# Performance work log

Hardware: AMD Instinct MI355X
Metric: run time of the kernel (lower is better)

Reference implementation:

```python
import jax, jax.numpy as jnp
import numpy as np

AGENT_SIZE = 64
NEIGH_SIZE = 64
NUM_HEAD = 4
MID_SIZE = 32
N_AGENT = 200000
HM = NUM_HEAD * MID_SIZE  # 128
OUT = HM // 2             # 64


def _xavier(key, shape):
    fan_in, fan_out = shape[0], shape[1]
    std = (2.0 / (fan_in + fan_out)) ** 0.5
    return jax.random.normal(key, shape, dtype=jnp.float32) * std


def setup_inputs() -> dict:
    key = jax.random.key(0)
    ks = jax.random.split(key, 12)
    agent = jax.random.normal(ks[0], (N_AGENT, AGENT_SIZE), dtype=jnp.float32)
    neighbor = jax.random.normal(ks[1], (N_AGENT, 4, NEIGH_SIZE), dtype=jnp.float32)
    neighbor_mask = jax.random.randint(ks[2], (N_AGENT, 4), 0, 2, dtype=jnp.int32)
    return {
        "agent": agent,
        "neighbor": neighbor,
        "neighbor_mask": neighbor_mask,
        "W_agent": _xavier(ks[3], (AGENT_SIZE, HM)),
        "b_agent": jnp.zeros((HM,), jnp.float32),
        "W_neigh": _xavier(ks[4], (NEIGH_SIZE, HM)),
        "b_neigh": jnp.zeros((HM,), jnp.float32),
        "W_hid": _xavier(ks[5], (NEIGH_SIZE, HM)),
        "b_hid": jnp.zeros((HM,), jnp.float32),
        "W_out": _xavier(ks[6], (HM, OUT)),
        "b_out": jnp.zeros((OUT,), jnp.float32),
    }


def reference(agent, neighbor, neighbor_mask,
              W_agent, b_agent, W_neigh, b_neigh,
              W_hid, b_hid, W_out, b_out):
    n = agent.shape[0]
    mask = neighbor_mask.astype(jnp.float32)  # [n, 4], 1 = masked
    # linear + relu projections
    a = jax.nn.relu(agent @ W_agent + b_agent).reshape(n, NUM_HEAD, MID_SIZE)          # [n,h,m]
    nr = jax.nn.relu(neighbor @ W_neigh + b_neigh).reshape(n, 4, NUM_HEAD, MID_SIZE)   # [n,4,h,m]
    nh = jax.nn.relu(neighbor @ W_hid + b_hid).reshape(n, 4, NUM_HEAD, MID_SIZE)       # [n,4,h,m]
    # attention logits: agent . neighbor per head -> [n, h, 4]
    att = jnp.einsum('nhm,nkhm->nhk', a, nr)
    att_score = jax.nn.softmax(mask[:, None, :] * -1e8 + att, axis=-1)                 # [n,h,4]
    att_score = (1.0 - mask[:, None, :]) * att_score
    # weighted MEAN over the 4 neighbors (faithful to .mean(2))
    out = jnp.einsum('nhk,nkhm->nhm', att_score, nh) / 4.0                              # [n,h,m]
    out = out.reshape(n, HM)
    return jax.nn.relu(out @ W_out + b_out)
```

## Files before the change

### kernel.cpp

```cpp
#include <hip/hip_runtime.h>
#include <cstdint>


typedef _Float16 f16;
typedef f16 f16x8 __attribute__((ext_vector_type(8)));
typedef float f32x4 __attribute__((ext_vector_type(4)));

#define MFMA(a, b, c) __builtin_amdgcn_mfma_f32_16x16x32_f16(a, b, c, 0, 0, 0)

__device__ __forceinline__ f16x8 ld_cvt8(const float* __restrict__ p) {
    float4 a = *(const float4*)p;
    float4 b = *(const float4*)(p + 4);
    f16x8 r;
    r[0] = (f16)a.x; r[1] = (f16)a.y; r[2] = (f16)a.z; r[3] = (f16)a.w;
    r[4] = (f16)b.x; r[5] = (f16)b.y; r[6] = (f16)b.z; r[7] = (f16)b.w;
    return r;
}

__device__ __forceinline__ float rowsum16(float x) {
    x += __int_as_float(__builtin_amdgcn_update_dpp(0, __float_as_int(x), 0x128, 0xf, 0xf, true));
    x += __int_as_float(__builtin_amdgcn_update_dpp(0, __float_as_int(x), 0x124, 0xf, 0xf, true));
    x += __int_as_float(__builtin_amdgcn_update_dpp(0, __float_as_int(x), 0x122, 0xf, 0xf, true));
    x += __int_as_float(__builtin_amdgcn_update_dpp(0, __float_as_int(x), 0x121, 0xf, 0xf, true));
    return x;
}

__global__ void prep_w(const float* __restrict__ Wa, const float* __restrict__ Wn,
                       const float* __restrict__ Wh, const float* __restrict__ Wo,
                       f16* __restrict__ ws) {
    int i = blockIdx.x * 256 + threadIdx.x;
    int m = i >> 13;
    int j = i & 8191;
    if (m < 3) {
        const float* W = (m == 0) ? Wa : ((m == 1) ? Wn : Wh);
        int n = j >> 6, k = j & 63;
        ws[m * 8192 + j] = (f16)W[k * 128 + n];
    } else {
        int n = j >> 7, k = j & 127;
        ws[24576 + j] = (f16)Wo[k * 64 + n];
    }
}

__global__ __launch_bounds__(256, 4)
void gat_mfma(const float* __restrict__ agent,
              const float* __restrict__ neighbor,
              const int*   __restrict__ nmask,
              const f16*   __restrict__ ws,
              const float* __restrict__ ba, const float* __restrict__ bn,
              const float* __restrict__ bh, const float* __restrict__ bo,
              float* __restrict__ out)
{
    __shared__ float mneg[256];
    __shared__ f16   ot[64 * 136];

    const int tid  = threadIdx.x;
    const int lane = tid & 63;
    const int h    = __builtin_amdgcn_readfirstlane(tid >> 6);
    const int l15  = lane & 15;
    const int q    = lane >> 4;
    const long base = (long)blockIdx.x * 64;

    mneg[tid] = -1e8f * (float)nmask[base * 4 + tid];

    const float bav[2] = { ba[h * 32 + l15], ba[h * 32 + 16 + l15] };
    const float bnv[2] = { bn[h * 32 + l15], bn[h * 32 + 16 + l15] };
    const float bhv[2] = { bh[h * 32 + l15], bh[h * 32 + 16 + l15] };
    const float bov    = bo[h * 16 + l15];

    const f16* wsn = ws + 8192;
    const f16* wsh = ws + 16384;
    const f16* wso = ws + 24576;

    f16x8 wn[2][2], wh[2][2];
    #pragma unroll
    for (int ct = 0; ct < 2; ++ct)
        #pragma unroll
        for (int ks = 0; ks < 2; ++ks) {
            int n = h * 32 + ct * 16 + l15;
            wn[ct][ks] = *(const f16x8*)(wsn + n * 64 + ks * 32 + q * 8);
            wh[ct][ks] = *(const f16x8*)(wsh + n * 64 + ks * 32 + q * 8);
        }

    __syncthreads();

    #pragma unroll 1
    for (int rt = 0; rt < 4; ++rt) {
        f32x4 p0 = {0.f, 0.f, 0.f, 0.f}, p1 = {0.f, 0.f, 0.f, 0.f};
        {
            const float* ap = agent + (base + rt * 16 + l15) * 64 + q * 8;
            f16x8 a0 = ld_cvt8(ap);
            f16x8 a1 = ld_cvt8(ap + 32);
            #pragma unroll
            for (int ct = 0; ct < 2; ++ct) {
                f16x8 w0 = *(const f16x8*)(ws + (h * 32 + ct * 16 + l15) * 64 + q * 8);
                f16x8 w1 = *(const f16x8*)(ws + (h * 32 + ct * 16 + l15) * 64 + 32 + q * 8);
                f32x4 c = {0.f, 0.f, 0.f, 0.f};
                c = MFMA(a0, w0, c);
                c = MFMA(a1, w1, c);
                if (ct == 0) p0 = c; else p1 = c;
            }
            #pragma unroll
            for (int r = 0; r < 4; ++r) {
                p0[r] = fmaxf(p0[r] + bav[0], 0.f);
                p1[r] = fmaxf(p1[r] + bav[1], 0.f);
            }
        }

        f32x4 o0 = {0.f, 0.f, 0.f, 0.f}, o1 = {0.f, 0.f, 0.f, 0.f};
        f32x4 ls = {0.f, 0.f, 0.f, 0.f};
        #pragma unroll
        for (int k = 0; k < 4; ++k) {
            const float* nb = neighbor + ((base + rt * 16 + l15) * 4 + k) * 64 + q * 8;
            f16x8 a0 = ld_cvt8(nb);
            f16x8 a1 = ld_cvt8(nb + 32);
            f32x4 n0 = {0.f,0.f,0.f,0.f}, n1 = {0.f,0.f,0.f,0.f};
            f32x4 h0 = {0.f,0.f,0.f,0.f}, h1 = {0.f,0.f,0.f,0.f};
            n0 = MFMA(a0, wn[0][0], n0); n0 = MFMA(a1, wn[0][1], n0);
            n1 = MFMA(a0, wn[1][0], n1); n1 = MFMA(a1, wn[1][1], n1);
            h0 = MFMA(a0, wh[0][0], h0); h0 = MFMA(a1, wh[0][1], h0);
            h1 = MFMA(a0, wh[1][0], h1); h1 = MFMA(a1, wh[1][1], h1);
            #pragma unroll
            for (int r = 0; r < 4; ++r) {
                n0[r] = fmaxf(n0[r] + bnv[0], 0.f);
                n1[r] = fmaxf(n1[r] + bnv[1], 0.f);
                h0[r] = fmaxf(h0[r] + bhv[0], 0.f);
                h1[r] = fmaxf(h1[r] + bhv[1], 0.f);
            }
            #pragma unroll
            for (int r = 0; r < 4; ++r) {
                float tp = p0[r] * n0[r] + p1[r] * n1[r];
                float logit = rowsum16(tp);
                float s = logit + mneg[(rt * 16 + q * 4 + r) * 4 + k];
                float e = __expf(s);
                ls[r] += e;
                float ep = (s > -1e7f) ? e : 0.f;
                o0[r] += ep * h0[r];
                o1[r] += ep * h1[r];
            }
        }

        #pragma unroll
        for (int r = 0; r < 4; ++r) {
            float inv = 0.25f / (ls[r] + 1e-30f);
            int row = rt * 16 + q * 4 + r;
            ot[row * 136 + h * 32 + l15]      = (f16)(o0[r] * inv);
            ot[row * 136 + h * 32 + 16 + l15] = (f16)(o1[r] * inv);
        }
    }
    __syncthreads();

    f16x8 wof[4];
    #pragma unroll
    for (int ks = 0; ks < 4; ++ks)
        wof[ks] = *(const f16x8*)(wso + (h * 16 + l15) * 128 + ks * 32 + q * 8);
    #pragma unroll
    for (int rt = 0; rt < 4; ++rt) {
        f32x4 y = {0.f, 0.f, 0.f, 0.f};
        #pragma unroll
        for (int ks = 0; ks < 4; ++ks) {
            f16x8 of = *(const f16x8*)(ot + (rt * 16 + l15) * 136 + ks * 32 + q * 8);
            y = MFMA(of, wof[ks], y);
        }
        #pragma unroll
        for (int r = 0; r < 4; ++r)
            out[(base + rt * 16 + q * 4 + r) * 64 + h * 16 + l15] = fmaxf(y[r] + bov, 0.f);
    }
}

extern "C" void kernel_launch(void* const* d_in, const int* in_sizes, int n_in,
                              void* d_out, int out_size, void* d_ws, size_t ws_size,
                              hipStream_t stream) {
    const float* agent    = (const float*)d_in[0];
    const float* neighbor = (const float*)d_in[1];
    const int*   nmask    = (const int*)d_in[2];
    const float* Wa = (const float*)d_in[3];
    const float* ba = (const float*)d_in[4];
    const float* Wn = (const float*)d_in[5];
    const float* bn = (const float*)d_in[6];
    const float* Wh = (const float*)d_in[7];
    const float* bh = (const float*)d_in[8];
    const float* Wo = (const float*)d_in[9];
    const float* bo = (const float*)d_in[10];
    float* out = (float*)d_out;
    f16* ws = (f16*)d_ws;

    prep_w<<<128, 256, 0, stream>>>(Wa, Wn, Wh, Wo, ws);

    const int n = in_sizes[0] / 64;
    const int blocks = n / 64;
    gat_mfma<<<blocks, 256, 0, stream>>>(agent, neighbor, nmask, ws,
                                         ba, bn, bh, bo, out);
}
```

Before: 421.5 us.

## Stage agent and neighbor tiles cooperatively through swizzled LDS with register prefetch

After: 472.3 us. 12.0% more time.

```diff
diff --git a/kernel.cpp b/kernel.cpp
--- a/kernel.cpp
+++ b/kernel.cpp
@@ -4,18 +4,10 @@
 
 typedef _Float16 f16;
 typedef f16 f16x8 __attribute__((ext_vector_type(8)));
+typedef f16 f16x4 __attribute__((ext_vector_type(4)));
 typedef float f32x4 __attribute__((ext_vector_type(4)));
 
 #define MFMA(a, b, c) __builtin_amdgcn_mfma_f32_16x16x32_f16(a, b, c, 0, 0, 0)
-
-__device__ __forceinline__ f16x8 ld_cvt8(const float* __restrict__ p) {
-    float4 a = *(const float4*)p;
-    float4 b = *(const float4*)(p + 4);
-    f16x8 r;
-    r[0] = (f16)a.x; r[1] = (f16)a.y; r[2] = (f16)a.z; r[3] = (f16)a.w;
-    r[4] = (f16)b.x; r[5] = (f16)b.y; r[6] = (f16)b.z; r[7] = (f16)b.w;
-    return r;
-}
 
 __device__ __forceinline__ float rowsum16(float x) {
     x += __int_as_float(__builtin_amdgcn_update_dpp(0, __float_as_int(x), 0x128, 0xf, 0xf, true));
@@ -41,6 +33,10 @@
     }
 }
 
+__device__ __forceinline__ int swz(int row, int col) {
+    return row * 64 + (col ^ ((row & 7) << 3));
+}
+
 __global__ __launch_bounds__(256, 4)
 void gat_mfma(const float* __restrict__ agent,
               const float* __restrict__ neighbor,
@@ -51,6 +47,8 @@
               float* __restrict__ out)
 {
     __shared__ float mneg[256];
+    __shared__ f16   sa[16 * 64];
+    __shared__ f16   sn[64 * 64];
     __shared__ f16   ot[64 * 136];
 
     const int tid  = threadIdx.x;
@@ -81,28 +79,61 @@
             wh[ct][ks] = *(const f16x8*)(wsh + n * 64 + ks * 32 + q * 8);
         }
 
-    __syncthreads();
+    const int sr  = tid >> 4;
+    const int sc4 = (tid & 15) * 4;
+    const float* agp = agent    + base * 64;
+    const float* nbp = neighbor + base * 4 * 64;
+
+    float4 ra = *(const float4*)(agp + tid * 4);
+    float4 rn4[4];
+    #pragma unroll
+    for (int i = 0; i < 4; ++i)
+        rn4[i] = *(const float4*)(nbp + i * 1024 + tid * 4);
 
     #pragma unroll 1
     for (int rt = 0; rt < 4; ++rt) {
-        f32x4 p0 = {0.f, 0.f, 0.f, 0.f}, p1 = {0.f, 0.f, 0.f, 0.f};
+        __syncthreads();
+
+        f16x8 wa[2][2];
+        #pragma unroll
+        for (int ct = 0; ct < 2; ++ct)
+            #pragma unroll
+            for (int ks = 0; ks < 2; ++ks)
+                wa[ct][ks] = *(const f16x8*)(ws + (h * 32 + ct * 16 + l15) * 64 + ks * 32 + q * 8);
+
         {
-            const float* ap = agent + (base + rt * 16 + l15) * 64 + q * 8;
-            f16x8 a0 = ld_cvt8(ap);
-            f16x8 a1 = ld_cvt8(ap + 32);
-            #pragma unroll
-            for (int ct = 0; ct < 2; ++ct) {
-                f16x8 w0 = *(const f16x8*)(ws + (h * 32 + ct * 16 + l15) * 64 + q * 8);
-                f16x8 w1 = *(const f16x8*)(ws + (h * 32 + ct * 16 + l15) * 64 + 32 + q * 8);
-                f32x4 c = {0.f, 0.f, 0.f, 0.f};
-                c = MFMA(a0, w0, c);
-                c = MFMA(a1, w1, c);
-                if (ct == 0) p0 = c; else p1 = c;
-            }
+            f16x4 va = { (f16)ra.x, (f16)ra.y, (f16)ra.z, (f16)ra.w };
+            *(f16x4*)&sa[swz(sr, sc4)] = va;
+            #pragma unroll
+            for (int i = 0; i < 4; ++i) {
+                int rg = i * 16 + sr;
+                int lr = (rg & 3) * 16 + (rg >> 2);
+                f16x4 v = { (f16)rn4[i].x, (f16)rn4[i].y, (f16)rn4[i].z, (f16)rn4[i].w };
+                *(f16x4*)&sn[swz(lr, sc4)] = v;
+            }
+        }
+
+        {
+            int rtn = (rt < 3) ? rt + 1 : 3;
+            ra = *(const float4*)(agp + rtn * 1024 + tid * 4);
+            #pragma unroll
+            for (int i = 0; i < 4; ++i)
+                rn4[i] = *(const float4*)(nbp + rtn * 4096 + i * 1024 + tid * 4);
+        }
+
+        __syncthreads();
+
+        f32x4 p0 = { bav[0], bav[0], bav[0], bav[0] };
+        f32x4 p1 = { bav[1], bav[1], bav[1], bav[1] };
+        {
+            f16x8 a0 = *(const f16x8*)&sa[swz(l15, q * 8)];
+            f16x8 a1 = *(const f16x8*)&sa[swz(l15, 32 + q * 8)];
+            p0 = MFMA(a0, wa[0][0], p0); p0 = MFMA(a1, wa[0][1], p0);
+            p1 = MFMA(a0, wa[1][0], p1); p1 = MFMA(a1, wa[1][1], p1);
             #pragma unroll
             for (int r = 0; r < 4; ++r) {
-                p0[r] = fmaxf(p0[r] + bav[0], 0.f);
-                p1[r] = fmaxf(p1[r] + bav[1], 0.f);
+                p0[r] = fmaxf(p0[r], 0.f);
+                p1[r] = fmaxf(p1[r], 0.f);
             }
         }
 
@@ -110,21 +141,23 @@
         f32x4 ls = {0.f, 0.f, 0.f, 0.f};
         #pragma unroll
         for (int k = 0; k < 4; ++k) {
-            const float* nb = neighbor + ((base + rt * 16 + l15) * 4 + k) * 64 + q * 8;
-            f16x8 a0 = ld_cvt8(nb);
-            f16x8 a1 = ld_cvt8(nb + 32);
-            f32x4 n0 = {0.f,0.f,0.f,0.f}, n1 = {0.f,0.f,0.f,0.f};
-            f32x4 h0 = {0.f,0.f,0.f,0.f}, h1 = {0.f,0.f,0.f,0.f};
+            int lr = k * 16 + l15;
+            f16x8 a0 = *(const f16x8*)&sn[swz(lr, q * 8)];
+            f16x8 a1 = *(const f16x8*)&sn[swz(lr, 32 + q * 8)];
+            f32x4 n0 = { bnv[0], bnv[0], bnv[0], bnv[0] };
+            f32x4 n1 = { bnv[1], bnv[1], bnv[1], bnv[1] };
+            f32x4 h0 = { bhv[0], bhv[0], bhv[0], bhv[0] };
+            f32x4 h1 = { bhv[1], bhv[1], bhv[1], bhv[1] };
             n0 = MFMA(a0, wn[0][0], n0); n0 = MFMA(a1, wn[0][1], n0);
             n1 = MFMA(a0, wn[1][0], n1); n1 = MFMA(a1, wn[1][1], n1);
             h0 = MFMA(a0, wh[0][0], h0); h0 = MFMA(a1, wh[0][1], h0);
             h1 = MFMA(a0, wh[1][0], h1); h1 = MFMA(a1, wh[1][1], h1);
             #pragma unroll
             for (int r = 0; r < 4; ++r) {
-                n0[r] = fmaxf(n0[r] + bnv[0], 0.f);
-                n1[r] = fmaxf(n1[r] + bnv[1], 0.f);
-                h0[r] = fmaxf(h0[r] + bhv[0], 0.f);
-                h1[r] = fmaxf(h1[r] + bhv[1], 0.f);
+                n0[r] = fmaxf(n0[r], 0.f);
+                n1[r] = fmaxf(n1[r], 0.f);
+                h0[r] = fmaxf(h0[r], 0.f);
+                h1[r] = fmaxf(h1[r], 0.f);
             }
             #pragma unroll
             for (int r = 0; r < 4; ++r) {
@@ -133,9 +166,8 @@
                 float s = logit + mneg[(rt * 16 + q * 4 + r) * 4 + k];
                 float e = __expf(s);
                 ls[r] += e;
-                float ep = (s > -1e7f) ? e : 0.f;
-                o0[r] += ep * h0[r];
-                o1[r] += ep * h1[r];
+                o0[r] += e * h0[r];
+                o1[r] += e * h1[r];
             }
         }
 
@@ -155,7 +187,7 @@
         wof[ks] = *(const f16x8*)(wso + (h * 16 + l15) * 128 + ks * 32 + q * 8);
     #pragma unroll
     for (int rt = 0; rt < 4; ++rt) {
-        f32x4 y = {0.f, 0.f, 0.f, 0.f};
+        f32x4 y = { bov, bov, bov, bov };
         #pragma unroll
         for (int ks = 0; ks < 4; ++ks) {
             f16x8 of = *(const f16x8*)(ot + (rt * 16 + l15) * 136 + ks * 32 + q * 8);
@@ -163,7 +195,7 @@
         }
         #pragma unroll
         for (int r = 0; r < 4; ++r)
-            out[(base + rt * 16 + q * 4 + r) * 64 + h * 16 + l15] = fmaxf(y[r] + bov, 0.f);
+            out[(base + rt * 16 + q * 4 + r) * 64 + h * 16 + l15] = fmaxf(y[r], 0.f);
     }
 }
 
```
